# Kernel optimization log

Hardware: AMD Instinct MI355X
Metric: run time of the kernel (lower is better)

The kernel has to match this reference:

```python
import jax, jax.numpy as jnp
import numpy as np
import math

B, T, D = 2, 2048, 1024
H, HS = 16, 64  # n_heads, head_size; D == H*HS


def setup_inputs() -> dict:
    key = jax.random.key(0)
    k1, k2, k3 = jax.random.split(key, 3)
    x = jax.random.normal(k1, (B, T, D), dtype=jnp.float32)
    w_qkv = jax.random.normal(k2, (D, 3 * D), dtype=jnp.float32) * (1.0 / math.sqrt(D))
    b_qkv = jnp.zeros((3 * D,), dtype=jnp.float32)
    w_out = jax.random.normal(k3, (D, D), dtype=jnp.float32) * (1.0 / math.sqrt(D))
    b_out = jnp.zeros((D,), dtype=jnp.float32)
    return {"x": x, "w_qkv": w_qkv, "b_qkv": b_qkv, "w_out": w_out, "b_out": b_out}


def reference(x, w_qkv, b_qkv, w_out, b_out):
    b, t, d = x.shape
    qkv = x @ w_qkv + b_qkv                       # (B,T,3D)
    q, k, v = jnp.split(qkv, 3, axis=-1)
    # (B,T,D) -> (B,H,T,HS)
    q = q.reshape(b, t, H, HS).transpose(0, 2, 1, 3)
    k = k.reshape(b, t, H, HS).transpose(0, 2, 1, 3)
    v = v.reshape(b, t, H, HS).transpose(0, 2, 1, 3)
    scale = 1.0 / math.sqrt(HS)
    attn = jnp.einsum('bhqd,bhkd->bhqk', q, k) * scale  # (B,H,T,T)
    causal = jnp.tril(jnp.ones((t, t), dtype=bool))
    attn = jnp.where(causal[None, None], attn, -jnp.inf)
    attn = jax.nn.softmax(attn, axis=-1)
    o = jnp.einsum('bhqk,bhkd->bhqd', attn, v)          # (B,H,T,HS)
    o = o.transpose(0, 2, 1, 3).reshape(b, t, d)
    return o @ w_out + b_out
```

## Files before the change

kernel.cpp:

```cpp
#include <hip/hip_runtime.h>
#include <math.h>

#define B_  2
#define T_  2048
#define D_  1024
#define H_  16
#define HS_ 64
#define M_  (B_*T_)

typedef __bf16 bf16x8 __attribute__((ext_vector_type(8)));
typedef float  f32x4  __attribute__((ext_vector_type(4)));
typedef unsigned short u16;

static __device__ __forceinline__ u16 f2bf(float f) {
    __bf16 h = (__bf16)f;
    return *reinterpret_cast<u16*>(&h);
}

static __device__ __forceinline__ void glds16(const u16* g, u16* l) {
    __builtin_amdgcn_global_load_lds(
        (const __attribute__((address_space(1))) void*)g,
        (__attribute__((address_space(3))) void*)l, 16, 0, 0);
}

__global__ __launch_bounds__(256) void prep_kernel(
    const float* __restrict__ x, const float* __restrict__ w_qkv,
    const float* __restrict__ w_out,
    u16* __restrict__ Xb, u16* __restrict__ WqkvT, u16* __restrict__ WoutT)
{
    int bid = blockIdx.x;
    if (bid < 4096) {
        int i = (bid * 256 + threadIdx.x) * 4;
        float4 v = *reinterpret_cast<const float4*>(x + i);
        ushort4 o;
        o.x = f2bf(v.x); o.y = f2bf(v.y); o.z = f2bf(v.z); o.w = f2bf(v.w);
        *reinterpret_cast<ushort4*>(Xb + i) = o;
        return;
    }
    const float* in; u16* out; int C; int c0, r0;
    if (bid < 4096 + 3072) {
        int t = bid - 4096;
        in = w_qkv; out = WqkvT; C = 3 * D_;
        c0 = (t % 96) * 32; r0 = (t / 96) * 32;
    } else {
        int t = bid - 7168;
        in = w_out; out = WoutT; C = D_;
        c0 = (t & 31) * 32; r0 = (t >> 5) * 32;
    }
    __shared__ float tile[32][33];
    int tr = threadIdx.x >> 3, tc4 = (threadIdx.x & 7) * 4;
    float4 v = *reinterpret_cast<const float4*>(in + (size_t)(r0 + tr) * C + c0 + tc4);
    tile[tr][tc4+0] = v.x; tile[tr][tc4+1] = v.y;
    tile[tr][tc4+2] = v.z; tile[tr][tc4+3] = v.w;
    __syncthreads();
    ushort4 o;
    o.x = f2bf(tile[tc4+0][tr]); o.y = f2bf(tile[tc4+1][tr]);
    o.z = f2bf(tile[tc4+2][tr]); o.w = f2bf(tile[tc4+3][tr]);
    *reinterpret_cast<ushort4*>(out + (size_t)(c0 + tr) * D_ + r0 + tc4) = o;
}

__global__ __launch_bounds__(512, 2) void gemm_qkv(
    const u16* __restrict__ A, const u16* __restrict__ Bt,
    const float* __restrict__ bias,
    u16* __restrict__ Qb, u16* __restrict__ Kb, u16* __restrict__ Vt)
{
    constexpr int K  = D_;
    constexpr int NT = K / 64;

    __shared__ u16 LDS[2][2][2][8192];

    const int tid  = threadIdx.x;
    const int lane = tid & 63, wave = tid >> 6;
    const int wm = wave >> 2, wn = wave & 3;
    const int quad = lane >> 4, lr = lane & 15;

    const int lin = blockIdx.x + 16 * blockIdx.y;
    const int xcd = lin & 7, rr = lin >> 3;
    const int bm = (xcd & 3) * 4 + (rr & 3);
    const int bn = (xcd >> 2) * 6 + (rr >> 2);

    const u16* Ab = A  + (size_t)(bm * 256) * K;
    const u16* Bb = Bt + (size_t)(bn * 256) * K;

    const int r0 = tid >> 2;
    const int c0 = (tid & 3) ^ ((tid >> 3) & 3);
    const u16* sA0 = Ab + (size_t)r0 * K + c0 * 8;
    const u16* sA1 = sA0 + (size_t)128 * K;
    const u16* sB0 = Bb + (size_t)r0 * K + c0 * 8;
    const u16* sB1 = sB0 + (size_t)128 * K;
    const int d0 = tid * 8, d1 = (tid + 512) * 8;

    const int swz = (lr >> 1) & 3;
    const int eA = ((wm*128 + lr) * 4 + (quad ^ swz)) * 8;
    const int eB = ((wn*64  + lr) * 4 + (quad ^ swz)) * 8;

    f32x4 acc[8][4] = {};

#define STG(mat, kh, tt) do { \
        u16* _d = &LDS[(tt) & 1][mat][kh][0]; \
        const int _ko = (tt) * 64 + (kh) * 32; \
        glds16(((mat) ? sB0 : sA0) + _ko, _d + d0); \
        glds16(((mat) ? sB1 : sA1) + _ko, _d + d1); \
    } while (0)

#define MFMA_QUAD(mh) do { \
        __builtin_amdgcn_s_setprio(1); \
        _Pragma("unroll") \
        for (int i_ = 0; i_ < 4; ++i_) \
            _Pragma("unroll") \
            for (int j_ = 0; j_ < 4; ++j_) \
                acc[(mh)*4 + i_][j_] = __builtin_amdgcn_mfma_f32_16x16x32_bf16( \
                    a[i_], b[j_], acc[(mh)*4 + i_][j_], 0, 0, 0); \
        __builtin_amdgcn_s_setprio(0); \
    } while (0)

    STG(0,0,0); STG(1,0,0); STG(0,1,0); STG(1,1,0);
    asm volatile("s_waitcnt vmcnt(4)" ::: "memory");
    __builtin_amdgcn_s_barrier();

    for (int t = 0; t < NT; ++t) {
        const int cb = t & 1;
        const bool last = (t == NT - 1);
        const u16* Ar0 = &LDS[cb][0][0][0];
        const u16* Ar1 = &LDS[cb][0][1][0];
        const u16* Br0 = &LDS[cb][1][0][0];
        const u16* Br1 = &LDS[cb][1][1][0];
        bf16x8 a[4], b[4];

        #pragma unroll
        for (int i = 0; i < 4; ++i) a[i] = *reinterpret_cast<const bf16x8*>(Ar0 + eA + i*512);
        #pragma unroll
        for (int j = 0; j < 4; ++j) b[j] = *reinterpret_cast<const bf16x8*>(Br0 + eB + j*512);
        if (!last) STG(0,0,t+1);
        __builtin_amdgcn_s_barrier();
        asm volatile("s_waitcnt lgkmcnt(0)" ::: "memory");
        MFMA_QUAD(0);
        __builtin_amdgcn_s_barrier();

        #pragma unroll
        for (int i = 0; i < 4; ++i) a[i] = *reinterpret_cast<const bf16x8*>(Ar0 + eA + (i+4)*512);
        if (!last) STG(1,0,t+1);
        __builtin_amdgcn_s_barrier();
        asm volatile("s_waitcnt lgkmcnt(0)" ::: "memory");
        MFMA_QUAD(1);
        if (!last) { asm volatile("s_waitcnt vmcnt(4)" ::: "memory"); }
        else       { asm volatile("s_waitcnt vmcnt(0)" ::: "memory"); }
        __builtin_amdgcn_s_barrier();

        #pragma unroll
        for (int i = 0; i < 4; ++i) a[i] = *reinterpret_cast<const bf16x8*>(Ar1 + eA + i*512);
        #pragma unroll
        for (int j = 0; j < 4; ++j) b[j] = *reinterpret_cast<const bf16x8*>(Br1 + eB + j*512);
        if (!last) STG(0,1,t+1);
        __builtin_amdgcn_s_barrier();
        asm volatile("s_waitcnt lgkmcnt(0)" ::: "memory");
        MFMA_QUAD(0);
        __builtin_amdgcn_s_barrier();

        #pragma unroll
        for (int i = 0; i < 4; ++i) a[i] = *reinterpret_cast<const bf16x8*>(Ar1 + eA + (i+4)*512);
        if (!last) STG(1,1,t+1);
        __builtin_amdgcn_s_barrier();
        asm volatile("s_waitcnt lgkmcnt(0)" ::: "memory");
        MFMA_QUAD(1);
        asm volatile("s_waitcnt vmcnt(4)" ::: "memory");
        __builtin_amdgcn_s_barrier();
    }
#undef STG
#undef MFMA_QUAD

    #pragma unroll
    for (int i = 0; i < 8; ++i) {
        int m0 = bm*256 + wm*128 + i*16 + quad*4;
        #pragma unroll
        for (int j = 0; j < 4; ++j) {
            int ncol = bn*256 + wn*64 + j*16 + lr;
            float bv = bias[ncol];
            float v4[4];
            #pragma unroll
            for (int r = 0; r < 4; ++r) v4[r] = acc[i][j][r] + bv;
            int bb = m0 >> 11, t0 = m0 & (T_ - 1);
            int s = ncol >> 10, rem = ncol & 1023;
            int h = rem >> 6, d = rem & 63;
            int bh = bb * H_ + h;
            if (s == 0) {
                #pragma unroll
                for (int r = 0; r < 4; ++r)
                    Qb[((size_t)bh*T_ + t0 + r)*HS_ + d] = f2bf(v4[r] * 0.1803368801111244f);
            } else if (s == 1) {
                #pragma unroll
                for (int r = 0; r < 4; ++r)
                    Kb[((size_t)bh*T_ + t0 + r)*HS_ + d] = f2bf(v4[r]);
            } else {
                ushort4 o;
                o.x = f2bf(v4[0]); o.y = f2bf(v4[1]);
                o.z = f2bf(v4[2]); o.w = f2bf(v4[3]);
                *reinterpret_cast<ushort4*>(&Vt[((size_t)bh*HS_ + d)*T_ + t0]) = o;
            }
        }
    }
}

__global__ __launch_bounds__(256, 2) void gemm_out(
    const u16* __restrict__ A, const u16* __restrict__ Bt,
    const float* __restrict__ bias, float* __restrict__ Cf)
{
    constexpr int K  = D_;
    constexpr int N  = D_;
    constexpr int NT = K / 64;

    __shared__ u16 LDS[2][2][2][4096];

    const int tid  = threadIdx.x;
    const int lane = tid & 63, wave = tid >> 6;
    const int wm = wave >> 1, wn = wave & 1;
    const int quad = lane >> 4, lr = lane & 15;
    const int bm = blockIdx.x, bn = blockIdx.y;

    const u16* Ab = A  + (size_t)(bm * 128) * K;
    const u16* Bb = Bt + (size_t)(bn * 128) * K;

    const int r0 = tid >> 2;
    const int c0 = (tid & 3) ^ ((tid >> 3) & 3);
    const u16* sA0 = Ab + (size_t)r0 * K + c0 * 8;
    const u16* sA1 = sA0 + (size_t)64 * K;
    const u16* sB0 = Bb + (size_t)r0 * K + c0 * 8;
    const u16* sB1 = sB0 + (size_t)64 * K;
    const int d0 = tid * 8, d1 = (tid + 256) * 8;

    const int swz = (lr >> 1) & 3;
    const int eA = ((wm*64 + lr) * 4 + (quad ^ swz)) * 8;
    const int eB = ((wn*64 + lr) * 4 + (quad ^ swz)) * 8;

    f32x4 acc[4][4] = {};

#define STGO(kh, tt) do { \
        const int _ko = (tt) * 64 + (kh) * 32; \
        glds16(sA0 + _ko, &LDS[(tt) & 1][0][kh][0] + d0); \
        glds16(sA1 + _ko, &LDS[(tt) & 1][0][kh][0] + d1); \
        glds16(sB0 + _ko, &LDS[(tt) & 1][1][kh][0] + d0); \
        glds16(sB1 + _ko, &LDS[(tt) & 1][1][kh][0] + d1); \
    } while (0)

    STGO(0, 0); STGO(1, 0);
    asm volatile("s_waitcnt vmcnt(4)" ::: "memory");
    __builtin_amdgcn_s_barrier();

    for (int t = 0; t < NT; ++t) {
        const int cb = t & 1;
        const bool last = (t == NT - 1);
        bf16x8 a[4], b[4];

        {
            const u16* Ar = &LDS[cb][0][0][0];
            const u16* Br = &LDS[cb][1][0][0];
            #pragma unroll
            for (int i = 0; i < 4; ++i) a[i] = *reinterpret_cast<const bf16x8*>(Ar + eA + i*512);
            #pragma unroll
            for (int j = 0; j < 4; ++j) b[j] = *reinterpret_cast<const bf16x8*>(Br + eB + j*512);
            if (!last) STGO(0, t+1);
            __builtin_amdgcn_s_barrier();
            asm volatile("s_waitcnt lgkmcnt(0)" ::: "memory");
            __builtin_amdgcn_s_setprio(1);
            #pragma unroll
            for (int i = 0; i < 4; ++i)
                #pragma unroll
                for (int j = 0; j < 4; ++j)
                    acc[i][j] = __builtin_amdgcn_mfma_f32_16x16x32_bf16(a[i], b[j], acc[i][j], 0, 0, 0);
            __builtin_amdgcn_s_setprio(0);
            if (!last) { asm volatile("s_waitcnt vmcnt(4)" ::: "memory"); }
            else       { asm volatile("s_waitcnt vmcnt(0)" ::: "memory"); }
            __builtin_amdgcn_s_barrier();
        }

        {
            const u16* Ar = &LDS[cb][0][1][0];
            const u16* Br = &LDS[cb][1][1][0];
            #pragma unroll
            for (int i = 0; i < 4; ++i) a[i] = *reinterpret_cast<const bf16x8*>(Ar + eA + i*512);
            #pragma unroll
            for (int j = 0; j < 4; ++j) b[j] = *reinterpret_cast<const bf16x8*>(Br + eB + j*512);
            if (!last) STGO(1, t+1);
            __builtin_amdgcn_s_barrier();
            asm volatile("s_waitcnt lgkmcnt(0)" ::: "memory");
            __builtin_amdgcn_s_setprio(1);
            #pragma unroll
            for (int i = 0; i < 4; ++i)
                #pragma unroll
                for (int j = 0; j < 4; ++j)
                    acc[i][j] = __builtin_amdgcn_mfma_f32_16x16x32_bf16(a[i], b[j], acc[i][j], 0, 0, 0);
            __builtin_amdgcn_s_setprio(0);
            if (!last) { asm volatile("s_waitcnt vmcnt(4)" ::: "memory"); }
            __builtin_amdgcn_s_barrier();
        }
    }
#undef STGO

    #pragma unroll
    for (int i = 0; i < 4; ++i) {
        int m0 = bm*128 + wm*64 + i*16 + quad*4;
        #pragma unroll
        for (int j = 0; j < 4; ++j) {
            int ncol = bn*128 + wn*64 + j*16 + lr;
            float bv = bias[ncol];
            #pragma unroll
            for (int r = 0; r < 4; ++r)
                Cf[(size_t)(m0 + r) * N + ncol] = acc[i][j][r] + bv;
        }
    }
}

__global__ __launch_bounds__(256) void attn_kernel(
    const u16* __restrict__ Qb, const u16* __restrict__ Kb,
    const u16* __restrict__ Vt, u16* __restrict__ Ob)
{
    __shared__ u16 Ks[64 * 64];
    __shared__ u16 Vs[64 * 64];
    __shared__ u16 Ps[4][2][16 * 64];

    int tid  = threadIdx.x;
    int lane = tid & 63, wave = tid >> 6;
    int quad = lane >> 4, lr = lane & 15;

    int lin = blockIdx.x;
    int bh  = (lin & 7) + 8 * ((lin >> 3) & 3);
    int p   = lin >> 5;
    int qlo = p, qhi = 31 - p;
    int rlo = qlo * 64 + wave * 16;
    int rhi = qhi * 64 + wave * 16;

    const u16* QpL = Qb + ((size_t)bh * T_ + rlo) * HS_;
    const u16* QpH = Qb + ((size_t)bh * T_ + rhi) * HS_;
    bf16x8 qfL[2], qfH[2];
    #pragma unroll
    for (int h2 = 0; h2 < 2; ++h2) {
        qfL[h2] = *reinterpret_cast<const bf16x8*>(QpL + lr*HS_ + h2*32 + quad*8);
        qfH[h2] = *reinterpret_cast<const bf16x8*>(QpH + lr*HS_ + h2*32 + quad*8);
    }

    f32x4 OaL[4] = {}, OaH[4] = {};
    float lsumL = 0.f, lsumH = 0.f;

    int e   = quad ^ (lr & 7);
    int rb0 = (lr * 8 + e) * 8;
    int rb1 = (lr * 8 + (e ^ 4)) * 8;
    int off64[4];
    #pragma unroll
    for (int nt = 0; nt < 4; ++nt)
        off64[nt] = (lr*8 + ((2*nt + (quad >> 1)) ^ (lr & 7)))*8 + (quad & 1)*4;
    u16* PsL = Ps[wave][0];
    u16* PsH = Ps[wave][1];

    int srow = tid >> 3;
    int scol = ((tid & 7) ^ (srow & 7)) * 8;
    const u16* kp0 = Kb + ((size_t)bh*T_ + srow     )*HS_ + scol;
    const u16* kp1 = Kb + ((size_t)bh*T_ + srow + 32)*HS_ + scol;
    const u16* vp0 = Vt + ((size_t)bh*HS_ + srow     )*T_ + scol;
    const u16* vp1 = Vt + ((size_t)bh*HS_ + srow + 32)*T_ + scol;

    bf16x8 kpre0 = *reinterpret_cast<const bf16x8*>(kp0);
    bf16x8 kpre1 = *reinterpret_cast<const bf16x8*>(kp1);
    bf16x8 vpre0 = *reinterpret_cast<const bf16x8*>(vp0);
    bf16x8 vpre1 = *reinterpret_cast<const bf16x8*>(vp1);

    for (int jt = 0; jt <= qhi; ++jt) {
        __syncthreads();
        reinterpret_cast<bf16x8*>(Ks)[tid]       = kpre0;
        reinterpret_cast<bf16x8*>(Ks)[tid + 256] = kpre1;
        reinterpret_cast<bf16x8*>(Vs)[tid]       = vpre0;
        reinterpret_cast<bf16x8*>(Vs)[tid + 256] = vpre1;
        if (jt < qhi) {
            kp0 += 64*HS_; kp1 += 64*HS_; vp0 += 64; vp1 += 64;
            kpre0 = *reinterpret_cast<const bf16x8*>(kp0);
            kpre1 = *reinterpret_cast<const bf16x8*>(kp1);
            vpre0 = *reinterpret_cast<const bf16x8*>(vp0);
            vpre1 = *reinterpret_cast<const bf16x8*>(vp1);
        }
        __syncthreads();

        const bool lo = (jt <= qlo);

        f32x4 SaH[4] = {}, SaL[4] = {};
        __builtin_amdgcn_s_setprio(1);
        #pragma unroll
        for (int nt = 0; nt < 4; ++nt) {
            bf16x8 bk0 = *reinterpret_cast<const bf16x8*>(Ks + rb0 + nt*1024);
            bf16x8 bk1 = *reinterpret_cast<const bf16x8*>(Ks + rb1 + nt*1024);
            SaH[nt] = __builtin_amdgcn_mfma_f32_16x16x32_bf16(bk0, qfH[0], SaH[nt], 0, 0, 0);
            SaH[nt] = __builtin_amdgcn_mfma_f32_16x16x32_bf16(bk1, qfH[1], SaH[nt], 0, 0, 0);
            if (lo) {
                SaL[nt] = __builtin_amdgcn_mfma_f32_16x16x32_bf16(bk0, qfL[0], SaL[nt], 0, 0, 0);
                SaL[nt] = __builtin_amdgcn_mfma_f32_16x16x32_bf16(bk1, qfL[1], SaL[nt], 0, 0, 0);
            }
        }
        __builtin_amdgcn_s_setprio(0);

        if (jt == qhi) {
            #pragma unroll
            for (int nt = 0; nt < 4; ++nt)
                #pragma unroll
                for (int r = 0; r < 4; ++r) {
                    int kg = jt*64 + nt*16 + quad*4 + r;
                    int qg = rhi + lr;
                    if (kg > qg) SaH[nt][r] = -INFINITY;
                }
        }
        if (jt == qlo) {
            #pragma unroll
            for (int nt = 0; nt < 4; ++nt)
                #pragma unroll
                for (int r = 0; r < 4; ++r) {
                    int kg = jt*64 + nt*16 + quad*4 + r;
                    int qg = rlo + lr;
                    if (kg > qg) SaL[nt][r] = -INFINITY;
                }
        }

        #pragma unroll
        for (int nt = 0; nt < 4; ++nt) {
            float e0 = __builtin_amdgcn_exp2f(SaH[nt][0]);
            float e1 = __builtin_amdgcn_exp2f(SaH[nt][1]);
            float e2 = __builtin_amdgcn_exp2f(SaH[nt][2]);
            float e3 = __builtin_amdgcn_exp2f(SaH[nt][3]);
            lsumH += (e0 + e1) + (e2 + e3);
            ushort4 w;
            w.x = f2bf(e0); w.y = f2bf(e1); w.z = f2bf(e2); w.w = f2bf(e3);
            *reinterpret_cast<ushort4*>(PsH + off64[nt]) = w;
        }
        if (lo) {
            #pragma unroll
            for (int nt = 0; nt < 4; ++nt) {
                float e0 = __builtin_amdgcn_exp2f(SaL[nt][0]);
                float e1 = __builtin_amdgcn_exp2f(SaL[nt][1]);
                float e2 = __builtin_amdgcn_exp2f(SaL[nt][2]);
                float e3 = __builtin_amdgcn_exp2f(SaL[nt][3]);
                lsumL += (e0 + e1) + (e2 + e3);
                ushort4 w;
                w.x = f2bf(e0); w.y = f2bf(e1); w.z = f2bf(e2); w.w = f2bf(e3);
                *reinterpret_cast<ushort4*>(PsL + off64[nt]) = w;
            }
        }

        __builtin_amdgcn_s_setprio(1);
        #pragma unroll
        for (int kk = 0; kk < 2; ++kk) {
            int rb = kk ? rb1 : rb0;
            bf16x8 paH = *reinterpret_cast<const bf16x8*>(PsH + rb);
            bf16x8 paL = *reinterpret_cast<const bf16x8*>(PsL + rb);
            #pragma unroll
            for (int nt = 0; nt < 4; ++nt) {
                bf16x8 vb = *reinterpret_cast<const bf16x8*>(Vs + rb + nt*1024);
                OaH[nt] = __builtin_amdgcn_mfma_f32_16x16x32_bf16(paH, vb, OaH[nt], 0, 0, 0);
                if (lo)
                    OaL[nt] = __builtin_amdgcn_mfma_f32_16x16x32_bf16(paL, vb, OaL[nt], 0, 0, 0);
            }
        }
        __builtin_amdgcn_s_setprio(0);
    }

    int b = bh >> 4, h = bh & 15;
    float sH = lsumH;
    sH += __shfl_xor(sH, 16, 64);
    sH += __shfl_xor(sH, 32, 64);
    float sL = lsumL;
    sL += __shfl_xor(sL, 16, 64);
    sL += __shfl_xor(sL, 32, 64);
    #pragma unroll
    for (int r = 0; r < 4; ++r) {
        float invH = 1.f / __shfl(sH, quad*4 + r, 64);
        float invL = 1.f / __shfl(sL, quad*4 + r, 64);
        int qgH = rhi + quad*4 + r;
        int qgL = rlo + quad*4 + r;
        #pragma unroll
        for (int nt = 0; nt < 4; ++nt) {
            int d = nt*16 + lr;
            Ob[((size_t)b*T_ + qgH)*D_ + h*HS_ + d] = f2bf(OaH[nt][r] * invH);
            Ob[((size_t)b*T_ + qgL)*D_ + h*HS_ + d] = f2bf(OaL[nt][r] * invL);
        }
    }
}

extern "C" void kernel_launch(void* const* d_in, const int* in_sizes, int n_in,
                              void* d_out, int out_size, void* d_ws, size_t ws_size,
                              hipStream_t stream) {
    (void)in_sizes; (void)n_in; (void)out_size; (void)ws_size;
    const float* x     = (const float*)d_in[0];
    const float* w_qkv = (const float*)d_in[1];
    const float* b_qkv = (const float*)d_in[2];
    const float* w_out = (const float*)d_in[3];
    const float* b_out = (const float*)d_in[4];
    float* out = (float*)d_out;

    char* ws = (char*)d_ws;
    u16* Xb    = (u16*)ws; ws += (size_t)M_ * D_ * 2;
    u16* WqkvT = (u16*)ws; ws += (size_t)3 * D_ * D_ * 2;
    u16* WoutT = (u16*)ws; ws += (size_t)D_ * D_ * 2;
    u16* Qb    = (u16*)ws; ws += (size_t)M_ * D_ * 2;
    u16* Kb    = (u16*)ws; ws += (size_t)M_ * D_ * 2;
    u16* Vt    = (u16*)ws; ws += (size_t)M_ * D_ * 2;
    u16* Ob    = (u16*)ws; ws += (size_t)M_ * D_ * 2;

    prep_kernel<<<8192, 256, 0, stream>>>(x, w_qkv, w_out, Xb, WqkvT, WoutT);
    gemm_qkv<<<dim3(16, 12), 512, 0, stream>>>(
        Xb, WqkvT, b_qkv, Qb, Kb, Vt);
    attn_kernel<<<512, 256, 0, stream>>>(Qb, Kb, Vt, Ob);
    gemm_out<<<dim3(M_/128, D_/128), 256, 0, stream>>>(Ob, WoutT, b_out, out);
}
```

Baseline: 176.2 us.

## Triple-buffer K/V tiles and software-pipeline QK^T one tile ahead of softmax·V

Replaces the two-barrier-per-tile loop with a three-slot LDS ring for K and V plus a software pipeline. The QK^T MFMAs for tile j+1 are issued before the softmax and PV of tile j, and only one barrier is used per iteration. The aim is to overlap exp/softmax VALU work with MFMA and to hide global-to-LDS staging latency. In exchange it uses more LDS (three K/V buffers) and more live score registers, which could lower occupancy. The final tile is peeled out to apply the diagonal mask for the high query block.

```diff
diff --git a/kernel.cpp b/kernel.cpp
--- a/kernel.cpp
+++ b/kernel.cpp
@@ -314,8 +314,8 @@
     const u16* __restrict__ Qb, const u16* __restrict__ Kb,
     const u16* __restrict__ Vt, u16* __restrict__ Ob)
 {
-    __shared__ u16 Ks[64 * 64];
-    __shared__ u16 Vs[64 * 64];
+    __shared__ u16 Ks[3][64 * 64];
+    __shared__ u16 Vs[3][64 * 64];
     __shared__ u16 Ps[4][2][16 * 64];
 
     int tid  = threadIdx.x;
@@ -358,105 +358,136 @@
     const u16* vp0 = Vt + ((size_t)bh*HS_ + srow     )*T_ + scol;
     const u16* vp1 = Vt + ((size_t)bh*HS_ + srow + 32)*T_ + scol;
 
-    bf16x8 kpre0 = *reinterpret_cast<const bf16x8*>(kp0);
-    bf16x8 kpre1 = *reinterpret_cast<const bf16x8*>(kp1);
-    bf16x8 vpre0 = *reinterpret_cast<const bf16x8*>(vp0);
-    bf16x8 vpre1 = *reinterpret_cast<const bf16x8*>(vp1);
-
-    for (int jt = 0; jt <= qhi; ++jt) {
-        __syncthreads();
-        reinterpret_cast<bf16x8*>(Ks)[tid]       = kpre0;
-        reinterpret_cast<bf16x8*>(Ks)[tid + 256] = kpre1;
-        reinterpret_cast<bf16x8*>(Vs)[tid]       = vpre0;
-        reinterpret_cast<bf16x8*>(Vs)[tid + 256] = vpre1;
-        if (jt < qhi) {
-            kp0 += 64*HS_; kp1 += 64*HS_; vp0 += 64; vp1 += 64;
-            kpre0 = *reinterpret_cast<const bf16x8*>(kp0);
-            kpre1 = *reinterpret_cast<const bf16x8*>(kp1);
-            vpre0 = *reinterpret_cast<const bf16x8*>(vp0);
-            vpre1 = *reinterpret_cast<const bf16x8*>(vp1);
-        }
-        __syncthreads();
-
-        const bool lo = (jt <= qlo);
-
-        f32x4 SaH[4] = {}, SaL[4] = {};
-        __builtin_amdgcn_s_setprio(1);
-        #pragma unroll
-        for (int nt = 0; nt < 4; ++nt) {
-            bf16x8 bk0 = *reinterpret_cast<const bf16x8*>(Ks + rb0 + nt*1024);
-            bf16x8 bk1 = *reinterpret_cast<const bf16x8*>(Ks + rb1 + nt*1024);
-            SaH[nt] = __builtin_amdgcn_mfma_f32_16x16x32_bf16(bk0, qfH[0], SaH[nt], 0, 0, 0);
-            SaH[nt] = __builtin_amdgcn_mfma_f32_16x16x32_bf16(bk1, qfH[1], SaH[nt], 0, 0, 0);
-            if (lo) {
-                SaL[nt] = __builtin_amdgcn_mfma_f32_16x16x32_bf16(bk0, qfL[0], SaL[nt], 0, 0, 0);
-                SaL[nt] = __builtin_amdgcn_mfma_f32_16x16x32_bf16(bk1, qfL[1], SaL[nt], 0, 0, 0);
-            }
-        }
-        __builtin_amdgcn_s_setprio(0);
-
-        if (jt == qhi) {
-            #pragma unroll
-            for (int nt = 0; nt < 4; ++nt)
-                #pragma unroll
-                for (int r = 0; r < 4; ++r) {
-                    int kg = jt*64 + nt*16 + quad*4 + r;
-                    int qg = rhi + lr;
-                    if (kg > qg) SaH[nt][r] = -INFINITY;
-                }
-        }
-        if (jt == qlo) {
-            #pragma unroll
-            for (int nt = 0; nt < 4; ++nt)
-                #pragma unroll
-                for (int r = 0; r < 4; ++r) {
-                    int kg = jt*64 + nt*16 + quad*4 + r;
-                    int qg = rlo + lr;
-                    if (kg > qg) SaL[nt][r] = -INFINITY;
-                }
-        }
-
-        #pragma unroll
-        for (int nt = 0; nt < 4; ++nt) {
-            float e0 = __builtin_amdgcn_exp2f(SaH[nt][0]);
-            float e1 = __builtin_amdgcn_exp2f(SaH[nt][1]);
-            float e2 = __builtin_amdgcn_exp2f(SaH[nt][2]);
-            float e3 = __builtin_amdgcn_exp2f(SaH[nt][3]);
-            lsumH += (e0 + e1) + (e2 + e3);
-            ushort4 w;
-            w.x = f2bf(e0); w.y = f2bf(e1); w.z = f2bf(e2); w.w = f2bf(e3);
-            *reinterpret_cast<ushort4*>(PsH + off64[nt]) = w;
-        }
-        if (lo) {
-            #pragma unroll
-            for (int nt = 0; nt < 4; ++nt) {
-                float e0 = __builtin_amdgcn_exp2f(SaL[nt][0]);
-                float e1 = __builtin_amdgcn_exp2f(SaL[nt][1]);
-                float e2 = __builtin_amdgcn_exp2f(SaL[nt][2]);
-                float e3 = __builtin_amdgcn_exp2f(SaL[nt][3]);
-                lsumL += (e0 + e1) + (e2 + e3);
-                ushort4 w;
-                w.x = f2bf(e0); w.y = f2bf(e1); w.z = f2bf(e2); w.w = f2bf(e3);
-                *reinterpret_cast<ushort4*>(PsL + off64[nt]) = w;
-            }
-        }
-
-        __builtin_amdgcn_s_setprio(1);
-        #pragma unroll
-        for (int kk = 0; kk < 2; ++kk) {
-            int rb = kk ? rb1 : rb0;
-            bf16x8 paH = *reinterpret_cast<const bf16x8*>(PsH + rb);
-            bf16x8 paL = *reinterpret_cast<const bf16x8*>(PsL + rb);
-            #pragma unroll
-            for (int nt = 0; nt < 4; ++nt) {
-                bf16x8 vb = *reinterpret_cast<const bf16x8*>(Vs + rb + nt*1024);
-                OaH[nt] = __builtin_amdgcn_mfma_f32_16x16x32_bf16(paH, vb, OaH[nt], 0, 0, 0);
-                if (lo)
-                    OaL[nt] = __builtin_amdgcn_mfma_f32_16x16x32_bf16(paL, vb, OaL[nt], 0, 0, 0);
-            }
-        }
-        __builtin_amdgcn_s_setprio(0);
-    }
+    bf16x8 kpre0, kpre1, vpre0, vpre1;
+
+    u16 *KsV = Ks[0], *KsK = Ks[1], *KsW = Ks[2];
+    u16 *VsV = Vs[0], *VsK = Vs[1], *VsW = Vs[2];
+
+#define LOADREGS() do { \
+    kpre0 = *reinterpret_cast<const bf16x8*>(kp0); \
+    kpre1 = *reinterpret_cast<const bf16x8*>(kp1); \
+    vpre0 = *reinterpret_cast<const bf16x8*>(vp0); \
+    vpre1 = *reinterpret_cast<const bf16x8*>(vp1); \
+    kp0 += 64*HS_; kp1 += 64*HS_; vp0 += 64; vp1 += 64; } while (0)
+
+#define WRITEBUF(KD, VD) do { \
+    reinterpret_cast<bf16x8*>(KD)[tid]       = kpre0; \
+    reinterpret_cast<bf16x8*>(KD)[tid + 256] = kpre1; \
+    reinterpret_cast<bf16x8*>(VD)[tid]       = vpre0; \
+    reinterpret_cast<bf16x8*>(VD)[tid + 256] = vpre1; } while (0)
+
+#define QKC(SH, SL, KB, LOC) do { \
+    __builtin_amdgcn_s_setprio(1); \
+    _Pragma("unroll") \
+    for (int nt = 0; nt < 4; ++nt) { \
+        bf16x8 bk0 = *reinterpret_cast<const bf16x8*>((KB) + rb0 + nt*1024); \
+        bf16x8 bk1 = *reinterpret_cast<const bf16x8*>((KB) + rb1 + nt*1024); \
+        f32x4 z = {}; \
+        (SH)[nt] = __builtin_amdgcn_mfma_f32_16x16x32_bf16(bk0, qfH[0], z, 0, 0, 0); \
+        (SH)[nt] = __builtin_amdgcn_mfma_f32_16x16x32_bf16(bk1, qfH[1], (SH)[nt], 0, 0, 0); \
+        if (LOC) { \
+            (SL)[nt] = __builtin_amdgcn_mfma_f32_16x16x32_bf16(bk0, qfL[0], z, 0, 0, 0); \
+            (SL)[nt] = __builtin_amdgcn_mfma_f32_16x16x32_bf16(bk1, qfL[1], (SL)[nt], 0, 0, 0); \
+        } \
+    } \
+    __builtin_amdgcn_s_setprio(0); } while (0)
+
+#define SMPV(SH, SL, jj, LOC) do { \
+    if ((LOC) && (jj) == qlo) { \
+        _Pragma("unroll") \
+        for (int nt = 0; nt < 4; ++nt) \
+            _Pragma("unroll") \
+            for (int r = 0; r < 4; ++r) { \
+                int kg = (jj)*64 + nt*16 + quad*4 + r; \
+                if (kg > rlo + lr) (SL)[nt][r] = -INFINITY; \
+            } \
+    } \
+    _Pragma("unroll") \
+    for (int nt = 0; nt < 4; ++nt) { \
+        float e0 = __builtin_amdgcn_exp2f((SH)[nt][0]); \
+        float e1 = __builtin_amdgcn_exp2f((SH)[nt][1]); \
+        float e2 = __builtin_amdgcn_exp2f((SH)[nt][2]); \
+        float e3 = __builtin_amdgcn_exp2f((SH)[nt][3]); \
+        lsumH += (e0 + e1) + (e2 + e3); \
+        ushort4 w; w.x = f2bf(e0); w.y = f2bf(e1); w.z = f2bf(e2); w.w = f2bf(e3); \
+        *reinterpret_cast<ushort4*>(PsH + off64[nt]) = w; \
+    } \
+    if (LOC) { \
+        _Pragma("unroll") \
+        for (int nt = 0; nt < 4; ++nt) { \
+            float e0 = __builtin_amdgcn_exp2f((SL)[nt][0]); \
+            float e1 = __builtin_amdgcn_exp2f((SL)[nt][1]); \
+            float e2 = __builtin_amdgcn_exp2f((SL)[nt][2]); \
+            float e3 = __builtin_amdgcn_exp2f((SL)[nt][3]); \
+            lsumL += (e0 + e1) + (e2 + e3); \
+            ushort4 w; w.x = f2bf(e0); w.y = f2bf(e1); w.z = f2bf(e2); w.w = f2bf(e3); \
+            *reinterpret_cast<ushort4*>(PsL + off64[nt]) = w; \
+        } \
+    } \
+    __builtin_amdgcn_s_setprio(1); \
+    _Pragma("unroll") \
+    for (int kk = 0; kk < 2; ++kk) { \
+        int rb = kk ? rb1 : rb0; \
+        bf16x8 paH = *reinterpret_cast<const bf16x8*>(PsH + rb); \
+        bf16x8 paL = paH; \
+        if (LOC) paL = *reinterpret_cast<const bf16x8*>(PsL + rb); \
+        _Pragma("unroll") \
+        for (int nt = 0; nt < 4; ++nt) { \
+            bf16x8 vb = *reinterpret_cast<const bf16x8*>(VsV + rb + nt*1024); \
+            OaH[nt] = __builtin_amdgcn_mfma_f32_16x16x32_bf16(paH, vb, OaH[nt], 0, 0, 0); \
+            if (LOC) OaL[nt] = __builtin_amdgcn_mfma_f32_16x16x32_bf16(paL, vb, OaL[nt], 0, 0, 0); \
+        } \
+    } \
+    __builtin_amdgcn_s_setprio(0); } while (0)
+
+#define MASKH(SH) do { \
+    _Pragma("unroll") \
+    for (int nt = 0; nt < 4; ++nt) \
+        _Pragma("unroll") \
+        for (int r = 0; r < 4; ++r) { \
+            int kg = qhi*64 + nt*16 + quad*4 + r; \
+            if (kg > rhi + lr) (SH)[nt][r] = -INFINITY; \
+        } } while (0)
+
+#define ITER(SCH, SCL, SNH, SNL, jj) do { \
+    const bool loN_ = ((jj) + 1 <= qlo); \
+    const bool loC_ = ((jj) <= qlo); \
+    QKC(SNH, SNL, KsK, loN_); \
+    SMPV(SCH, SCL, (jj), loC_); \
+    if ((jj) + 2 <= qhi) { WRITEBUF(KsW, VsW); } \
+    if ((jj) + 3 <= qhi) { LOADREGS(); } \
+    asm volatile("s_waitcnt lgkmcnt(0)" ::: "memory"); \
+    __builtin_amdgcn_s_barrier(); \
+    { u16* t_ = KsV; KsV = KsK; KsK = KsW; KsW = t_; } \
+    { u16* t_ = VsV; VsV = VsK; VsK = VsW; VsW = t_; } \
+} while (0)
+
+    LOADREGS(); WRITEBUF(Ks[0], Vs[0]);
+    LOADREGS(); WRITEBUF(Ks[1], Vs[1]);
+    LOADREGS();
+    asm volatile("s_waitcnt lgkmcnt(0)" ::: "memory");
+    __builtin_amdgcn_s_barrier();
+
+    f32x4 SAH[4], SAL[4], SBH[4], SBL[4];
+    QKC(SAH, SAL, Ks[0], true);
+
+    int j = 0;
+    for (; j + 2 <= qhi; j += 2) {
+        ITER(SAH, SAL, SBH, SBL, j);
+        ITER(SBH, SBL, SAH, SAL, j + 1);
+    }
+    bool curA = true;
+    if (j < qhi) { ITER(SAH, SAL, SBH, SBL, j); ++j; curA = false; }
+
+    if (curA) { MASKH(SAH); SMPV(SAH, SAL, -1, false); }
+    else      { MASKH(SBH); SMPV(SBH, SBL, -1, false); }
+
+#undef LOADREGS
+#undef WRITEBUF
+#undef QKC
+#undef SMPV
+#undef MASKH
+#undef ITER
 
     int b = bh >> 4, h = bh & 15;
     float sH = lsumH;
```

After: 204.5 us. +16.1%, slower.
